# Kernel optimization log

Measured on AMD Instinct MI355X. Metric: run time of the kernel, lower is better.

## Reference

```python
import jax, jax.numpy as jnp
import numpy as np

N_NODES = 100000


def setup_inputs() -> dict:
    key = jax.random.key(0)
    ks = jax.random.split(key, 9)
    E = 1600000
    x = jax.random.normal(ks[0], (N_NODES, 12), dtype=jnp.float32)
    edge_index = jax.random.randint(ks[1], (2, E), 0, N_NODES, dtype=jnp.int64)
    def glorot(k, shape):
        lim = float(np.sqrt(6.0 / (shape[0] + shape[1])))
        return jax.random.uniform(k, shape, jnp.float32, -lim, lim)
    return {
        "x": x,
        "edge_index": edge_index,
        "W1": glorot(ks[2], (12, 64)),
        "b1": jnp.zeros((64,), jnp.float32),
        "W2": glorot(ks[3], (64, 128)),
        "b2": jnp.zeros((128,), jnp.float32),
        "W3": glorot(ks[4], (128, 96)),
        "b3": jnp.zeros((96,), jnp.float32),
    }


def reference(x, edge_index, W1, b1, W2, b2, W3, b3):
    N = x.shape[0]
    F_channel, n_his = 8, 12
    src, dst = edge_index[0], edge_index[1]
    # add self loops (PyG GCNConv default)
    loop = jnp.arange(N, dtype=src.dtype)
    src = jnp.concatenate([src, loop])
    dst = jnp.concatenate([dst, loop])
    # symmetric normalization: norm_e = deg[src]^-1/2 * deg[dst]^-1/2
    deg = jax.ops.segment_sum(jnp.ones_like(src, dtype=x.dtype), dst, num_segments=N)
    dinv = jnp.where(deg > 0, jax.lax.rsqrt(deg), 0.0)
    norm = dinv[src] * dinv[dst]  # [E+N]

    def gcn(h, W, b):
        hw = h @ W  # transform first (out_ch <= in-edge fanout cost)
        agg = jax.ops.segment_sum(hw[src] * norm[:, None], dst, num_segments=N)
        return agg + b

    h = jax.nn.relu(gcn(x, W1, b1))
    h = jax.nn.relu(gcn(h, W2, b2))
    h = gcn(h, W3, b3)
    return h.reshape(N, F_channel, n_his)
```

## Files before the change

kernel.cpp:

```cpp
#include <hip/hip_runtime.h>
#include <hip/hip_bf16.h>
#include <hip/hip_fp16.h>


static inline int cdiv(int a, int b) { return (a + b - 1) / b; }
constexpr int BLOCK = 256;
constexpr int BSHIFT = 9;
constexpr int BNODES = 1 << BSHIFT;

typedef float nfloat4 __attribute__((ext_vector_type(4)));
typedef _Float16 f16x8 __attribute__((ext_vector_type(8)));
typedef float f32x16 __attribute__((ext_vector_type(16)));


__device__ __forceinline__ void nt_store_raw16(void* p, float4 v) {
    nfloat4 nv;
    nv.x = v.x; nv.y = v.y; nv.z = v.z; nv.w = v.w;
    __builtin_nontemporal_store(nv, (nfloat4*)p);
}

struct h4 { __half2 a, b; };
__device__ __forceinline__ void store_h4(__half* p, float4 v) {
    h4 r;
    r.a = __floats2half2_rn(v.x, v.y);
    r.b = __floats2half2_rn(v.z, v.w);
    *(h4*)p = r;
}

__device__ __forceinline__ void h8_add(float* acc, float4 raw) {
    union { float4 f; __half2 h[4]; } u;
    u.f = raw;
#pragma unroll
    for (int j = 0; j < 4; ++j) {
        float2 p = __half22float2(u.h[j]);
        acc[2 * j] += p.x;
        acc[2 * j + 1] += p.y;
    }
}


template <int CHUNK>
__global__ void bucket_count_kernel(const int* __restrict__ dst, int E,
                                    int* __restrict__ bcnt, int NB) {
    __shared__ int cnt[256];
    for (int i = threadIdx.x; i < NB; i += blockDim.x) cnt[i] = 0;
    __syncthreads();
    const int e0 = blockIdx.x * CHUNK;
    const int e1 = min(e0 + CHUNK, E);
    for (int e = e0 + threadIdx.x; e < e1; e += blockDim.x)
        atomicAdd(&cnt[dst[e] >> BSHIFT], 1);
    __syncthreads();
    for (int i = threadIdx.x; i < NB; i += blockDim.x)
        if (cnt[i]) atomicAdd(&bcnt[i], cnt[i]);
}

__global__ void bucket_scan_kernel(const int* __restrict__ bcnt, int* __restrict__ gbase,
                                   int* __restrict__ gcur, int NB) {
    __shared__ int tmp[256];
    int t = threadIdx.x;
    int v = (t < NB) ? bcnt[t] : 0;
    tmp[t] = v;
    __syncthreads();
    for (int off = 1; off < 256; off <<= 1) {
        int add = (t >= off) ? tmp[t - off] : 0;
        __syncthreads();
        tmp[t] += add;
        __syncthreads();
    }
    if (t < NB) { int ex = tmp[t] - v; gbase[t] = ex; gcur[t] = ex; }
}

template <int CHUNK>
__global__ void bin_edges_kernel(const int* __restrict__ ei, int E,
                                 int* __restrict__ gcur, unsigned* __restrict__ binned,
                                 int NB) {
    __shared__ int cnt[256], base[256], rk[256];
    for (int i = threadIdx.x; i < NB; i += blockDim.x) { cnt[i] = 0; rk[i] = 0; }
    __syncthreads();
    const int e0 = blockIdx.x * CHUNK;
    const int e1 = min(e0 + CHUNK, E);
    for (int e = e0 + threadIdx.x; e < e1; e += blockDim.x)
        atomicAdd(&cnt[ei[E + e] >> BSHIFT], 1);
    __syncthreads();
    for (int i = threadIdx.x; i < NB; i += blockDim.x)
        base[i] = atomicAdd(&gcur[i], cnt[i]);
    __syncthreads();
    for (int e = e0 + threadIdx.x; e < e1; e += blockDim.x) {
        int s = ei[e], d = ei[E + e];
        int b = d >> BSHIFT;
        int r = atomicAdd(&rk[b], 1);
        binned[base[b] + r] = (unsigned)s | ((unsigned)(d & (BNODES - 1)) << 17);
    }
}

__global__ void csr_fill_kernel(const int* __restrict__ gbase, const int* __restrict__ bcnt,
                                const unsigned* __restrict__ binned,
                                int* __restrict__ deg, float* __restrict__ dinv,
                                int* __restrict__ row_ptr, int* __restrict__ csr_src,
                                int* __restrict__ dh, int N) {
    __shared__ int c[BNODES];
    __shared__ int ps[256];
    __shared__ int dhloc[64];
    const int t = threadIdx.x;
    const int b = blockIdx.x;
    const int node0 = b << BSHIFT;
    if (t < BNODES) c[t] = 0;
    if (t < 64) dhloc[t] = 0;
    __syncthreads();
    const int base = gbase[b];
    const int end = base + bcnt[b];
    for (int e = base + t; e < end; e += 1024)
        atomicAdd(&c[binned[e] >> 17], 1);
    __syncthreads();
    int s0 = 0, s1 = 0;
    if (t < 256) {
        s0 = c[2 * t]; s1 = c[2 * t + 1];
        ps[t] = s0 + s1;
    }
    __syncthreads();
    for (int off = 1; off < 256; off <<= 1) {
        int add = (t >= off && t < 256) ? ps[t - off] : 0;
        __syncthreads();
        if (t < 256) ps[t] += add;
        __syncthreads();
    }
    if (t < 256) {
        const int ex = ps[t] - (s0 + s1);
        const int p0 = base + ex;
        const int p1 = p0 + s0;
        const int n0 = node0 + 2 * t;
        if (n0 < N) {
            row_ptr[n0] = p0; deg[n0] = s0; dinv[n0] = rsqrtf((float)s0 + 1.0f);
            atomicAdd(&dhloc[min(s0, 63)], 1);
            if (n0 + 1 < N) {
                row_ptr[n0 + 1] = p1; deg[n0 + 1] = s1; dinv[n0 + 1] = rsqrtf((float)s1 + 1.0f);
                atomicAdd(&dhloc[min(s1, 63)], 1);
            }
        }
        c[2 * t] = p0; c[2 * t + 1] = p1;
    }
    __syncthreads();
    if (t < 64 && dhloc[t]) atomicAdd(&dh[t], dhloc[t]);
    for (int e = base + t; e < end; e += 1024) {
        unsigned sd = binned[e];
        int pos = atomicAdd(&c[sd >> 17], 1);
        csr_src[pos] = (int)(sd & 0x1FFFFu);
    }
}


__global__ void dscan_kernel(int* __restrict__ dh) {
    __shared__ int tmp[64];
    int t = threadIdx.x;
    int v = dh[t];
    tmp[t] = v;
    __syncthreads();
    for (int off = 1; off < 64; off <<= 1) {
        int add = (t >= off) ? tmp[t - off] : 0;
        __syncthreads();
        tmp[t] += add;
        __syncthreads();
    }
    dh[t] = tmp[t] - v;
}

__global__ void dperm_kernel(const int* __restrict__ deg, const int* __restrict__ row_ptr,
                             const float* __restrict__ dinv, int* __restrict__ dh,
                             int4* __restrict__ hdr, int N) {
    __shared__ int cnt[64], base[64], rk[64];
    const int t = threadIdx.x;
    if (t < 64) { cnt[t] = 0; rk[t] = 0; }
    __syncthreads();
    const int i = blockIdx.x * blockDim.x + t;
    const int d = (i < N) ? deg[i] : 0;
    const int myb = (i < N) ? min(d, 63) : -1;
    if (myb >= 0) atomicAdd(&cnt[myb], 1);
    __syncthreads();
    if (t < 64) base[t] = cnt[t] ? atomicAdd(&dh[t], cnt[t]) : 0;
    __syncthreads();
    if (myb >= 0) {
        int r = atomicAdd(&rk[myb], 1);
        int slot = base[myb] + r;
        int4 h;
        h.x = row_ptr[i];
        h.y = d;
        h.z = i;
        h.w = __float_as_int(dinv[i]);
        hdr[N - 1 - slot] = h;
    }
}


__global__ void prescale_h_kernel(const float* __restrict__ x, const float* __restrict__ dinv,
                                  __half* __restrict__ xs, int N) {
    int i = blockIdx.x * blockDim.x + threadIdx.x;
    if (i >= N) return;
    float di = dinv[i];
    const float4* xr = (const float4*)(x + (size_t)i * 12);
    float4 a = xr[0], b = xr[1], c = xr[2];
    union { float4 f; __half2 h[4]; } u0, u1;
    u0.h[0] = __floats2half2_rn(a.x * di, a.y * di);
    u0.h[1] = __floats2half2_rn(a.z * di, a.w * di);
    u0.h[2] = __floats2half2_rn(b.x * di, b.y * di);
    u0.h[3] = __floats2half2_rn(b.z * di, b.w * di);
    u1.h[0] = __floats2half2_rn(c.x * di, c.y * di);
    u1.h[1] = __floats2half2_rn(c.z * di, c.w * di);
    u1.h[2] = __floats2half2_rn(0.f, 0.f);
    u1.h[3] = __floats2half2_rn(0.f, 0.f);
    float4* op = (float4*)(xs + (size_t)i * 16);
    op[0] = u0.f;
    op[1] = u1.f;
}


__global__ void gather_x_t1_kernel(const int4* __restrict__ hdr,
                                   const int* __restrict__ csr_src,
                                   const __half* __restrict__ xs,
                                   const float* __restrict__ W1,
                                   const float* __restrict__ b1,
                                   __half* __restrict__ h1h, int N) {
    __shared__ float W1s[12 * 64];
    __shared__ float xrow[128][12];
    const int tid = threadIdx.x;
    for (int u = tid; u < 12 * 64 / 4; u += 256)
        ((float4*)W1s)[u] = ((const float4*)W1)[u];

    const int t = blockIdx.x * 256 + tid;
    const bool valid = (t < N * 2);
    const int slot = t >> 1;
    const int c = t & 1;
    const int nl = tid >> 1;
    int4 H = valid ? hdr[slot] : make_int4(0, 0, 0, 0);
    const int* __restrict__ sp = csr_src + H.x;
    const int n = valid ? H.y : 0;
    const int i = H.z;
    const float di = __int_as_float(H.w);
    const int f0 = c * 8;

    float acc[8];
    {
        union { float4 f; __half2 h[4]; } u;
        u.f = *(const float4*)(xs + (size_t)i * 16 + f0);
#pragma unroll
        for (int j = 0; j < 4; ++j) {
            float2 p = __half22float2(u.h[j]);
            acc[2 * j] = p.x; acc[2 * j + 1] = p.y;
        }
    }

    int k = 0;
    if (n >= 8) {
        int s[8];
#pragma unroll
        for (int j = 0; j < 8; ++j) s[j] = sp[j];
        for (; k + 16 <= n; k += 8) {
            int ns[8];
#pragma unroll
            for (int j = 0; j < 8; ++j) ns[j] = sp[k + 8 + j];
            float4 v[8];
#pragma unroll
            for (int j = 0; j < 8; ++j) v[j] = *(const float4*)(xs + (size_t)s[j] * 16 + f0);
#pragma unroll
            for (int j = 0; j < 8; ++j) h8_add(acc, v[j]);
#pragma unroll
            for (int j = 0; j < 8; ++j) s[j] = ns[j];
        }
        float4 v[8];
#pragma unroll
        for (int j = 0; j < 8; ++j) v[j] = *(const float4*)(xs + (size_t)s[j] * 16 + f0);
#pragma unroll
        for (int j = 0; j < 8; ++j) h8_add(acc, v[j]);
        k += 8;
    }
    for (; k + 4 <= n; k += 4) {
        int s0 = sp[k + 0], s1 = sp[k + 1], s2 = sp[k + 2], s3 = sp[k + 3];
        float4 v0 = *(const float4*)(xs + (size_t)s0 * 16 + f0);
        float4 v1 = *(const float4*)(xs + (size_t)s1 * 16 + f0);
        float4 v2 = *(const float4*)(xs + (size_t)s2 * 16 + f0);
        float4 v3 = *(const float4*)(xs + (size_t)s3 * 16 + f0);
        h8_add(acc, v0); h8_add(acc, v1); h8_add(acc, v2); h8_add(acc, v3);
    }
    for (; k < n; ++k) {
        float4 v = *(const float4*)(xs + (size_t)sp[k] * 16 + f0);
        h8_add(acc, v);
    }

    if (valid) {
        if (c == 0) {
#pragma unroll
            for (int j = 0; j < 8; ++j) xrow[nl][j] = acc[j] * di;
        } else {
#pragma unroll
            for (int j = 0; j < 4; ++j) xrow[nl][8 + j] = acc[j] * di;
        }
    }
    __syncthreads();
    if (!valid) return;

    float xr[12];
#pragma unroll
    for (int j = 0; j < 12; ++j) xr[j] = xrow[nl][j];

    __half* op = h1h + (size_t)i * 64 + c * 32;
#pragma unroll
    for (int g = 0; g < 8; ++g) {
        const int c0 = c * 32 + g * 4;
        float4 r = *(const float4*)(b1 + c0);
#pragma unroll
        for (int kk = 0; kk < 12; ++kk) {
            const float4 w = *(const float4*)(W1s + kk * 64 + c0);
            r.x = fmaf(xr[kk], w.x, r.x);
            r.y = fmaf(xr[kk], w.y, r.y);
            r.z = fmaf(xr[kk], w.z, r.z);
            r.w = fmaf(xr[kk], w.w, r.w);
        }
        r.x = fmaxf(r.x, 0.f) * di; r.y = fmaxf(r.y, 0.f) * di;
        r.z = fmaxf(r.z, 0.f) * di; r.w = fmaxf(r.w, 0.f) * di;
        store_h4(op + g * 4, r);
    }
}


__global__ void prep_w_kernel(const float* __restrict__ W2, const float* __restrict__ W3,
                              __half* __restrict__ W2T, __half* __restrict__ W3T) {
    int i = blockIdx.x * 256 + threadIdx.x;
    if (i < 64 * 128) {
        int k = i >> 7, n = i & 127;
        W2T[n * 64 + k] = __float2half(W2[i]);
    } else {
        int j = i - 64 * 128;
        if (j < 128 * 96) {
            int k = j / 96, n = j - k * 96;
            W3T[n * 128 + k] = __float2half(W3[j]);
        }
    }
}

__global__ void fused_t2t3_kernel(const __half* __restrict__ agg1,
                                  const __half* __restrict__ W2T,
                                  const float* __restrict__ b2,
                                  const __half* __restrict__ W3T,
                                  const float* __restrict__ dinv,
                                  __half* __restrict__ out,
                                  int N) {
    constexpr int LDH = 136;
    __shared__ _Float16 h2s[4][32 * LDH];
    const int lane = threadIdx.x & 63;
    const int wid = threadIdx.x >> 6;
    const int l31 = lane & 31;
    const int lh = lane >> 5;
    _Float16* hs = h2s[wid];

    float b2v[4];
#pragma unroll
    for (int nt = 0; nt < 4; ++nt) b2v[nt] = b2[nt * 32 + l31];

    const int NT = N >> 5;
    for (int t = blockIdx.x * 4 + wid; t < NT; t += gridDim.x * 4) {
        const int r0 = t << 5;

        f16x8 a2[4];
#pragma unroll
        for (int kb = 0; kb < 4; ++kb)
            a2[kb] = *(const f16x8*)(agg1 + (size_t)(r0 + l31) * 64 + kb * 16 + lh * 8);
#pragma unroll
        for (int nt = 0; nt < 4; ++nt) {
            f32x16 c = {0.f, 0.f, 0.f, 0.f, 0.f, 0.f, 0.f, 0.f,
                        0.f, 0.f, 0.f, 0.f, 0.f, 0.f, 0.f, 0.f};
#pragma unroll
            for (int kb = 0; kb < 4; ++kb) {
                f16x8 b = *(const f16x8*)(W2T + (size_t)(nt * 32 + l31) * 64 + kb * 16 + lh * 8);
                c = __builtin_amdgcn_mfma_f32_32x32x16_f16(a2[kb], b, c, 0, 0, 0);
            }
#pragma unroll
            for (int r = 0; r < 16; ++r) {
                int row = (r & 3) + 8 * (r >> 2) + 4 * lh;
                float v = fmaxf(c[r] + b2v[nt], 0.f);
                hs[row * LDH + nt * 32 + l31] = (_Float16)v;
            }
        }

        f16x8 a3[8];
#pragma unroll
        for (int kb = 0; kb < 8; ++kb)
            a3[kb] = *(const f16x8*)(hs + l31 * LDH + kb * 16 + lh * 8);
        float4 dv[4];
#pragma unroll
        for (int rg = 0; rg < 4; ++rg)
            dv[rg] = *(const float4*)(dinv + r0 + rg * 8 + lh * 4);
#pragma unroll
        for (int nt = 0; nt < 3; ++nt) {
            f32x16 c = {0.f, 0.f, 0.f, 0.f, 0.f, 0.f, 0.f, 0.f,
                        0.f, 0.f, 0.f, 0.f, 0.f, 0.f, 0.f, 0.f};
#pragma unroll
            for (int kb = 0; kb < 8; ++kb) {
                f16x8 b = *(const f16x8*)(W3T + (size_t)(nt * 32 + l31) * 128 + kb * 16 + lh * 8);
                c = __builtin_amdgcn_mfma_f32_32x32x16_f16(a3[kb], b, c, 0, 0, 0);
            }
#pragma unroll
            for (int r = 0; r < 16; ++r) {
                int row = (r & 3) + 8 * (r >> 2) + 4 * lh;
                float dvv = ((const float*)&dv[r >> 2])[r & 3];
                hs[row * LDH + nt * 32 + l31] = (_Float16)(c[r] * dvv);
            }
        }

#pragma unroll
        for (int it = 0; it < 6; ++it) {
            int id = lane + it * 64;
            int row = id / 12, ch = id - row * 12;
            float4 v = *(const float4*)(hs + row * LDH + ch * 8);
            *(float4*)((char*)(out + (size_t)r0 * 96) + (size_t)id * 16) = v;
        }
    }
}


template <int F, bool HAS_BIAS, bool OUT_HALF>
__global__ void gather_h_kernel(const int4* __restrict__ hdr, const int* __restrict__ csr_src,
                                const __half* __restrict__ hws,
                                const float* __restrict__ b, void* __restrict__ out_v, int N) {
    constexpr int TPN = F / 8;
    int t = blockIdx.x * blockDim.x + threadIdx.x;
    if (t >= N * TPN) return;
    int slot = t / TPN;
    int c = t - slot * TPN;
    const int4 H = hdr[slot];
    const int* __restrict__ sp = csr_src + H.x;
    const int n = H.y;
    const int i = H.z;
    const float di = __int_as_float(H.w);
    int f0 = c * 8;

    float acc[8];
    {
        union { float4 f; __half2 h[4]; } u;
        u.f = *(const float4*)(hws + (size_t)i * F + f0);
#pragma unroll
        for (int j = 0; j < 4; ++j) {
            float2 p = __half22float2(u.h[j]);
            acc[2 * j] = p.x; acc[2 * j + 1] = p.y;
        }
    }

    int k = 0;
    if (n >= 8) {
        int s[8];
#pragma unroll
        for (int j = 0; j < 8; ++j) s[j] = sp[j];
        for (; k + 16 <= n; k += 8) {
            int ns[8];
#pragma unroll
            for (int j = 0; j < 8; ++j) ns[j] = sp[k + 8 + j];
            float4 v[8];
#pragma unroll
            for (int j = 0; j < 8; ++j) v[j] = *(const float4*)(hws + (size_t)s[j] * F + f0);
#pragma unroll
            for (int j = 0; j < 8; ++j) h8_add(acc, v[j]);
#pragma unroll
            for (int j = 0; j < 8; ++j) s[j] = ns[j];
        }
        float4 v[8];
#pragma unroll
        for (int j = 0; j < 8; ++j) v[j] = *(const float4*)(hws + (size_t)s[j] * F + f0);
#pragma unroll
        for (int j = 0; j < 8; ++j) h8_add(acc, v[j]);
        k += 8;
    }
    for (; k + 4 <= n; k += 4) {
        int s0 = sp[k + 0], s1 = sp[k + 1], s2 = sp[k + 2], s3 = sp[k + 3];
        float4 v0 = *(const float4*)(hws + (size_t)s0 * F + f0);
        float4 v1 = *(const float4*)(hws + (size_t)s1 * F + f0);
        float4 v2 = *(const float4*)(hws + (size_t)s2 * F + f0);
        float4 v3 = *(const float4*)(hws + (size_t)s3 * F + f0);
        h8_add(acc, v0); h8_add(acc, v1); h8_add(acc, v2); h8_add(acc, v3);
    }
    for (; k < n; ++k) {
        float4 v = *(const float4*)(hws + (size_t)sp[k] * F + f0);
        h8_add(acc, v);
    }

    float4 r0, r1;
    if (HAS_BIAS) {
        const float4 bb0 = *(const float4*)(b + f0);
        const float4 bb1 = *(const float4*)(b + f0 + 4);
        r0.x = fmaf(acc[0], di, bb0.x); r0.y = fmaf(acc[1], di, bb0.y);
        r0.z = fmaf(acc[2], di, bb0.z); r0.w = fmaf(acc[3], di, bb0.w);
        r1.x = fmaf(acc[4], di, bb1.x); r1.y = fmaf(acc[5], di, bb1.y);
        r1.z = fmaf(acc[6], di, bb1.z); r1.w = fmaf(acc[7], di, bb1.w);
    } else {
        r0.x = acc[0] * di; r0.y = acc[1] * di; r0.z = acc[2] * di; r0.w = acc[3] * di;
        r1.x = acc[4] * di; r1.y = acc[5] * di; r1.z = acc[6] * di; r1.w = acc[7] * di;
    }
    if (OUT_HALF) {
        union { float4 f; __half2 h[4]; } u;
        u.h[0] = __floats2half2_rn(r0.x, r0.y);
        u.h[1] = __floats2half2_rn(r0.z, r0.w);
        u.h[2] = __floats2half2_rn(r1.x, r1.y);
        u.h[3] = __floats2half2_rn(r1.z, r1.w);
        nt_store_raw16((__half*)out_v + (size_t)i * F + f0, u.f);
    } else {
        float* op = (float*)out_v + (size_t)i * F + f0;
        nt_store_raw16(op, r0);
        nt_store_raw16(op + 4, r1);
    }
}


extern "C" void kernel_launch(void* const* d_in, const int* in_sizes, int n_in,
                              void* d_out, int out_size, void* d_ws, size_t ws_size,
                              hipStream_t stream) {
    const float* x  = (const float*)d_in[0];
    const int*   ei = (const int*)d_in[1];
    const float* W1 = (const float*)d_in[2];
    const float* b1 = (const float*)d_in[3];
    const float* W2 = (const float*)d_in[4];
    const float* b2 = (const float*)d_in[5];
    const float* W3 = (const float*)d_in[6];
    const float* b3 = (const float*)d_in[7];
    float* out = (float*)d_out;

    const int N = in_sizes[0] / 12;
    const int E = in_sizes[1] / 2;
    const int NB = cdiv(N, BNODES);

    char* ws = (char*)d_ws;
    int*   deg     = (int*)ws;    ws += (size_t)N * sizeof(int);
    int*   row_ptr = (int*)ws;    ws += (size_t)N * sizeof(int);
    int*   bcnt    = (int*)ws;    ws += 256 * sizeof(int);
    int*   dh      = (int*)ws;    ws += 64 * sizeof(int);
    int*   gbase   = (int*)ws;    ws += 256 * sizeof(int);
    int*   gcur    = (int*)ws;    ws += 256 * sizeof(int);
    float* dinv    = (float*)ws;  ws += (size_t)N * sizeof(float);
    int4*  hdr     = (int4*)ws;   ws += (size_t)N * sizeof(int4);
    __half* W2Th   = (__half*)ws; ws += 128 * 64 * sizeof(__half);
    __half* W3Th   = (__half*)ws; ws += 96 * 128 * sizeof(__half);
    int*   csr_src = (int*)ws;    ws += (size_t)E * sizeof(int);
    float* bufA    = (float*)ws;  ws += (size_t)N * 128 * sizeof(float);
    float* bufB    = (float*)ws;
    unsigned* binned = (unsigned*)bufB;

    hipMemsetAsync(bcnt, 0, (256 + 64) * sizeof(int), stream);
    prep_w_kernel<<<80, 256, 0, stream>>>(W2, W3, W2Th, W3Th);
    bucket_count_kernel<8192><<<cdiv(E, 8192), BLOCK, 0, stream>>>(ei + E, E, bcnt, NB);
    bucket_scan_kernel<<<1, 256, 0, stream>>>(bcnt, gbase, gcur, NB);
    bin_edges_kernel<8192><<<cdiv(E, 8192), BLOCK, 0, stream>>>(ei, E, gcur, binned, NB);
    csr_fill_kernel<<<NB, 1024, 0, stream>>>(gbase, bcnt, binned, deg, dinv, row_ptr,
                                             csr_src, dh, N);

    dscan_kernel<<<1, 64, 0, stream>>>(dh);
    dperm_kernel<<<cdiv(N, BLOCK), BLOCK, 0, stream>>>(deg, row_ptr, dinv, dh, hdr, N);

    prescale_h_kernel<<<cdiv(N, BLOCK), BLOCK, 0, stream>>>(x, dinv, (__half*)bufA, N);
    gather_x_t1_kernel<<<cdiv(N * 2, BLOCK), BLOCK, 0, stream>>>(
        hdr, csr_src, (const __half*)bufA, W1, b1, (__half*)bufB, N);

    gather_h_kernel<64, false, true><<<cdiv(N * 8, BLOCK), BLOCK, 0, stream>>>(
        hdr, csr_src, (const __half*)bufB, nullptr, bufA, N);

    fused_t2t3_kernel<<<cdiv(N / 32, 4), 256, 0, stream>>>(
        (const __half*)bufA, W2Th, b2, W3Th, dinv, (__half*)bufB, N);

    gather_h_kernel<96, true, false><<<cdiv(N * 12, BLOCK), BLOCK, 0, stream>>>(
        hdr, csr_src, (const __half*)bufB, b3, out, N);
}
```

Baseline: 329.4 us.

## Fuse layer-2 neighbor gather into the MFMA transform kernel

Folds the 64-wide neighbor aggregation directly into the fused layer-2/layer-3 transform kernel. Each half-wave lane gathers and sums half of its row's neighbor features in registers, scales by dinv and feeds the result straight to MFMA, dropping one kernel launch and the agg1 round trip through global memory. In exchange, the gather loses the degree-permuted load balancing of the separate kernel: each lane walks its own row's neighbor list serially, so wavefronts can diverge on uneven degrees. The 32-float accumulator also raises register pressure, which is bounded with launch_bounds(256,3).

```diff
diff --git a/kernel.cpp b/kernel.cpp
--- a/kernel.cpp
+++ b/kernel.cpp
@@ -336,13 +336,15 @@
     }
 }
 
-__global__ void fused_t2t3_kernel(const __half* __restrict__ agg1,
-                                  const __half* __restrict__ W2T,
-                                  const float* __restrict__ b2,
-                                  const __half* __restrict__ W3T,
-                                  const float* __restrict__ dinv,
-                                  __half* __restrict__ out,
-                                  int N) {
+__global__ void __launch_bounds__(256, 3)
+fused_g64_t2t3_kernel(const __half* __restrict__ h1h,
+                      const int* __restrict__ row_ptr, const int* __restrict__ deg,
+                      const int* __restrict__ csr_src, const float* __restrict__ dinv,
+                      const __half* __restrict__ W2T,
+                      const float* __restrict__ b2,
+                      const __half* __restrict__ W3T,
+                      __half* __restrict__ out,
+                      int N) {
     constexpr int LDH = 136;
     __shared__ _Float16 h2s[4][32 * LDH];
     const int lane = threadIdx.x & 63;
@@ -358,11 +360,59 @@
     const int NT = N >> 5;
     for (int t = blockIdx.x * 4 + wid; t < NT; t += gridDim.x * 4) {
         const int r0 = t << 5;
-
+        const int i = r0 + l31;
+
+        float acc[32];
+        {
+            const char* rp = (const char*)h1h + (size_t)i * 128 + lh * 16;
+#pragma unroll
+            for (int kb = 0; kb < 4; ++kb) {
+                union { float4 f; __half2 h[4]; } u;
+                u.f = *(const float4*)(rp + kb * 32);
+#pragma unroll
+                for (int j = 0; j < 4; ++j) {
+                    float2 p = __half22float2(u.h[j]);
+                    acc[kb * 8 + 2 * j] = p.x;
+                    acc[kb * 8 + 2 * j + 1] = p.y;
+                }
+            }
+        }
+        {
+            const int* __restrict__ sp = csr_src + row_ptr[i];
+            const int n = deg[i];
+            if (n > 0) {
+                int s = sp[0];
+                int k = 0;
+                for (; k + 1 < n; ++k) {
+                    int s2 = sp[k + 1];
+                    const char* p = (const char*)h1h + (size_t)s * 128 + lh * 16;
+                    float4 v0 = *(const float4*)(p);
+                    float4 v1 = *(const float4*)(p + 32);
+                    float4 v2 = *(const float4*)(p + 64);
+                    float4 v3 = *(const float4*)(p + 96);
+                    h8_add(acc + 0, v0); h8_add(acc + 8, v1);
+                    h8_add(acc + 16, v2); h8_add(acc + 24, v3);
+                    s = s2;
+                }
+                const char* p = (const char*)h1h + (size_t)s * 128 + lh * 16;
+                float4 v0 = *(const float4*)(p);
+                float4 v1 = *(const float4*)(p + 32);
+                float4 v2 = *(const float4*)(p + 64);
+                float4 v3 = *(const float4*)(p + 96);
+                h8_add(acc + 0, v0); h8_add(acc + 8, v1);
+                h8_add(acc + 16, v2); h8_add(acc + 24, v3);
+            }
+        }
         f16x8 a2[4];
-#pragma unroll
-        for (int kb = 0; kb < 4; ++kb)
-            a2[kb] = *(const f16x8*)(agg1 + (size_t)(r0 + l31) * 64 + kb * 16 + lh * 8);
+        {
+            const float di = dinv[i];
+#pragma unroll
+            for (int kb = 0; kb < 4; ++kb)
+#pragma unroll
+                for (int j = 0; j < 8; ++j)
+                    a2[kb][j] = (_Float16)(acc[kb * 8 + j] * di);
+        }
+
 #pragma unroll
         for (int nt = 0; nt < 4; ++nt) {
             f32x16 c = {0.f, 0.f, 0.f, 0.f, 0.f, 0.f, 0.f, 0.f,
@@ -555,12 +605,10 @@
     gather_x_t1_kernel<<<cdiv(N * 2, BLOCK), BLOCK, 0, stream>>>(
         hdr, csr_src, (const __half*)bufA, W1, b1, (__half*)bufB, N);
 
-    gather_h_kernel<64, false, true><<<cdiv(N * 8, BLOCK), BLOCK, 0, stream>>>(
-        hdr, csr_src, (const __half*)bufB, nullptr, bufA, N);
-
-    fused_t2t3_kernel<<<cdiv(N / 32, 4), 256, 0, stream>>>(
-        (const __half*)bufA, W2Th, b2, W3Th, dinv, (__half*)bufB, N);
+    fused_g64_t2t3_kernel<<<cdiv(N / 32, 4), 256, 0, stream>>>(
+        (const __half*)bufB, row_ptr, deg, csr_src, dinv, W2Th, b2, W3Th,
+        (__half*)bufA, N);
 
     gather_h_kernel<96, true, false><<<cdiv(N * 12, BLOCK), BLOCK, 0, stream>>>(
-        hdr, csr_src, (const __half*)bufB, b3, out, N);
-}
+        hdr, csr_src, (const __half*)bufA, b3, out, N);
+}
```

Measured after the change: 326.4 us. Within noise of the previous version (-0.9%).
